# Optimization experiments

Hardware: AMD Instinct MI355X
Metric: run time of the kernel (lower is better)

The kernel has to match this reference:

```python
import jax, jax.numpy as jnp
import numpy as np

SQ, SK, D = 8192, 8192, 128

def setup_inputs() -> dict:
    k = jax.random.key(0)
    kq, kk, kv = jax.random.split(k, 3)
    query = jax.random.normal(kq, (SQ, D), dtype=jnp.float32)
    key = jax.random.normal(kk, (SK, D), dtype=jnp.float32)
    value = jax.random.normal(kv, (SK, D), dtype=jnp.float32)
    return {"query": query, "key": key, "value": value}

def reference(query, key, value):
    # attn_weights = dot_general(q, k, contract last dims) -> [Sq, Sk]
    attn_weights = jnp.einsum('qd,kd->qk', query, key)
    # softmax over key dims (second half of attn_weights dims)
    attn_weights = jax.nn.softmax(attn_weights, axis=-1)
    # dropout is identity: train=False -> deterministic
    # y = dot_general(attn_weights, value, contract key dims) -> [Sq, Dv]
    y = jnp.einsum('qk,kd->qd', attn_weights, value)
    return y
```

## Files before the change

kernel.cpp:

```cpp
#include <hip/hip_runtime.h>
#include <hip/hip_bf16.h>
#include <stdint.h>

#define SQ 8192
#define SK 8192
#define DH 128
#define L2E 1.4426950408889634f
#define CB 40.0f

typedef __attribute__((ext_vector_type(8))) _Float16 f16x8;
typedef __attribute__((ext_vector_type(8))) short bf16x8;
typedef __attribute__((ext_vector_type(16))) float f32x16;
typedef __attribute__((ext_vector_type(4))) short s16x4;
typedef __attribute__((ext_vector_type(4))) unsigned int u32x4;

__device__ __forceinline__ short f2h(float f) {
  _Float16 h = (_Float16)f;
  return __builtin_bit_cast(short, h);
}
__device__ __forceinline__ short f2bf(float f) {
  uint32_t u = __builtin_bit_cast(uint32_t, f);
  u = (u + 0x7FFFu + ((u >> 16) & 1u)) >> 16;
  return (short)u;
}

__device__ __forceinline__ void gl_lds16(const void* g, void* l) {
  __builtin_amdgcn_global_load_lds(
      (const __attribute__((address_space(1))) void*)g,
      (__attribute__((address_space(3))) void*)l, 16, 0, 0);
}

__global__ __launch_bounds__(256) void prep_kernel(const float* __restrict__ K,
                                                   const float* __restrict__ V,
                                                   short* __restrict__ Kimg,
                                                   short* __restrict__ Vimg) {
  __shared__ short T[32][136];
  const int tid = threadIdx.x;
  if (blockIdx.x < 256) {
    const int kb = blockIdx.x;
#pragma unroll
    for (int i = 0; i < 2; ++i) {
      int ci = i * 256 + tid;
      int kc = ci >> 6, lane = ci & 63;
      int key = kb * 32 + (lane & 31);
      int k0 = kc * 16 + (lane >> 5) * 8;
      const float* src = K + (size_t)key * DH + k0;
      float4 a = *(const float4*)src;
      float4 b = *(const float4*)(src + 4);
      s16x4 o0, o1;
      o0.x = f2h(a.x); o0.y = f2h(a.y); o0.z = f2h(a.z); o0.w = f2h(a.w);
      o1.x = f2h(b.x); o1.y = f2h(b.y); o1.z = f2h(b.z); o1.w = f2h(b.w);
      s16x4* dst = (s16x4*)(Kimg + (size_t)kb * 4096 + ci * 8);
      dst[0] = o0; dst[1] = o1;
    }
  } else {
    const int kb = blockIdx.x - 256;
#pragma unroll
    for (int i = 0; i < 4; ++i) {
      int fi = i * 256 + tid;
      int key = fi >> 5;
      int dc = (fi & 31) * 4;
      float4 v = ((const float4*)V)[(size_t)(kb * 32 + key) * (DH / 4) + (fi & 31)];
      T[key][dc + 0] = f2bf(v.x); T[key][dc + 1] = f2bf(v.y);
      T[key][dc + 2] = f2bf(v.z); T[key][dc + 3] = f2bf(v.w);
    }
    __syncthreads();
#pragma unroll
    for (int i = 0; i < 2; ++i) {
      int ci = i * 256 + tid;
      int lane = ci & 63;
      int g = ci >> 6;
      int dt = g & 3, ks = g >> 2;
      int base = ks * 16 + (lane >> 5) * 4;
      int d = dt * 32 + (lane & 31);
      s16x4 o0, o1;
      o0.x = T[base + 0][d]; o0.y = T[base + 1][d];
      o0.z = T[base + 2][d]; o0.w = T[base + 3][d];
      o1.x = T[base + 8][d]; o1.y = T[base + 9][d];
      o1.z = T[base + 10][d]; o1.w = T[base + 11][d];
      s16x4* dst = (s16x4*)(Vimg + (size_t)kb * 4096 + ci * 8);
      dst[0] = o0; dst[1] = o1;
    }
  }
}

#define NIT4 32
__global__ __launch_bounds__(512, 2) void attn_q128(const float* __restrict__ Q,
                                                    const short* __restrict__ Kimg,
                                                    const short* __restrict__ Vimg,
                                                    float* __restrict__ Opart,
                                                    float* __restrict__ lpart) {
  __shared__ __align__(16) char smem[98304];
  short* stg = (short*)smem;
  const int tid = threadIdx.x;
  const int w = tid >> 6;
  const int lane = tid & 63;
  const int half = lane >> 5;
  const int l32 = lane & 31;
  const int qh = w >> 1;
  const int kw = w & 1;
  const int b = blockIdx.x;
  const int kh = b & 3;
  const int qb = b >> 2;
  const int qrow0 = qb * 128 + qh * 32;
  const int kb0 = kh * 64;

  f16x8 qf[8];
  {
    const float* qp = Q + (size_t)(qrow0 + l32) * DH + half * 8;
#pragma unroll
    for (int kc = 0; kc < 8; ++kc) {
      float4 a = *(const float4*)(qp + kc * 16);
      float4 b2 = *(const float4*)(qp + kc * 16 + 4);
      f16x8 h;
      h[0] = (_Float16)a.x; h[1] = (_Float16)a.y; h[2] = (_Float16)a.z; h[3] = (_Float16)a.w;
      h[4] = (_Float16)b2.x; h[5] = (_Float16)b2.y; h[6] = (_Float16)b2.z; h[7] = (_Float16)b2.w;
      qf[kc] = h;
    }
  }

  f32x16 of[4];
#pragma unroll
  for (int dt = 0; dt < 4; ++dt)
#pragma unroll
    for (int c = 0; c < 16; ++c) of[dt][c] = 0.f;
  float l_lane = 0.f;

  const short* gsrc = (w < 4 ? Kimg : Vimg) + (size_t)kb0 * 4096 + (w & 3) * 2048 + lane * 8;
  const int ldso = ((w < 4) ? 0 : 8192) + (w & 3) * 2048;

  auto STAGE = [&](int c, int t) {
    const short* g = gsrc + (size_t)t * 8192;
    short* l = stg + c * 16384 + ldso;
#pragma unroll
    for (int j = 0; j < 4; ++j)
      gl_lds16(g + j * 512, l + j * 512);
  };

  STAGE(0, 0);
  STAGE(1, 1);
  asm volatile("s_waitcnt vmcnt(4)" ::: "memory");
  __builtin_amdgcn_s_barrier();
  __builtin_amdgcn_sched_barrier(0);

  for (int t = 0; t < NIT4; ++t) {
    const int cur = t % 3;
    const short* bk = stg + cur * 16384 + kw * 4096 + lane * 8;
    f16x8 kf[8];
#pragma unroll
    for (int kc = 0; kc < 8; ++kc) kf[kc] = *(const f16x8*)(bk + kc * 512);

    if (t + 2 < NIT4) STAGE((t + 2) % 3, t + 2);

    f32x16 sacc;
#pragma unroll
    for (int c = 0; c < 16; ++c) sacc[c] = 0.f;
#pragma unroll
    for (int kc = 0; kc < 8; ++kc)
      sacc = __builtin_amdgcn_mfma_f32_32x32x16_f16(kf[kc], qf[kc], sacc, 0, 0, 0);

    const short* bv = stg + cur * 16384 + 8192 + kw * 4096 + lane * 8;
    bf16x8 vf[8];
#pragma unroll
    for (int g2 = 0; g2 < 8; ++g2) vf[g2] = *(const bf16x8*)(bv + g2 * 512);

    u32x4 pav0, pav1;
#pragma unroll
    for (int r = 0; r < 4; ++r) {
      float pA = __builtin_amdgcn_exp2f(fmaf(sacc[2 * r], L2E, -CB));
      float pB = __builtin_amdgcn_exp2f(fmaf(sacc[2 * r + 1], L2E, -CB));
      float pC = __builtin_amdgcn_exp2f(fmaf(sacc[8 + 2 * r], L2E, -CB));
      float pD = __builtin_amdgcn_exp2f(fmaf(sacc[8 + 2 * r + 1], L2E, -CB));
      l_lane += (pA + pB) + (pC + pD);
      uint32_t uA = __builtin_bit_cast(uint32_t, pA); uA += 0x7FFFu + ((uA >> 16) & 1u);
      uint32_t uB = __builtin_bit_cast(uint32_t, pB); uB += 0x7FFFu + ((uB >> 16) & 1u);
      uint32_t uC = __builtin_bit_cast(uint32_t, pC); uC += 0x7FFFu + ((uC >> 16) & 1u);
      uint32_t uD = __builtin_bit_cast(uint32_t, pD); uD += 0x7FFFu + ((uD >> 16) & 1u);
      pav0[r] = __builtin_amdgcn_perm(uB, uA, 0x07060302u);
      pav1[r] = __builtin_amdgcn_perm(uD, uC, 0x07060302u);
    }
    bf16x8 pa0 = __builtin_bit_cast(bf16x8, pav0);
    bf16x8 pa1 = __builtin_bit_cast(bf16x8, pav1);

#pragma unroll
    for (int dt = 0; dt < 4; ++dt) {
      of[dt] = __builtin_amdgcn_mfma_f32_32x32x16_bf16(pa0, vf[dt], of[dt], 0, 0, 0);
      of[dt] = __builtin_amdgcn_mfma_f32_32x32x16_bf16(pa1, vf[4 + dt], of[dt], 0, 0, 0);
    }

    if (t + 1 < NIT4) {
      asm volatile("s_waitcnt vmcnt(4)" ::: "memory");
      __builtin_amdgcn_s_barrier();
      __builtin_amdgcn_sched_barrier(0);
    }
  }

  float l_tot = l_lane + __shfl_xor(l_lane, 32);

  __syncthreads();
  float* mO = (float*)smem;
  float* R = mO + qh * 4224;
  if (kw == 0) {
#pragma unroll
    for (int c = 0; c < 16; ++c) {
      const int row = (c & 3) + 8 * (c >> 2) + 4 * half;
      float* br = R + row * 132;
#pragma unroll
      for (int dt = 0; dt < 4; ++dt) br[dt * 32 + l32] = of[dt][c];
    }
    if (half == 0) R[l32 * 132 + 128] = l_tot;
  }
  __syncthreads();
  if (kw == 1) {
#pragma unroll
    for (int c = 0; c < 16; ++c) {
      const int row = (c & 3) + 8 * (c >> 2) + 4 * half;
      float* br = R + row * 132;
#pragma unroll
      for (int dt = 0; dt < 4; ++dt) br[dt * 32 + l32] += of[dt][c];
    }
    if (half == 0) R[l32 * 132 + 128] += l_tot;
  }
  __syncthreads();
  {
    const int row = tid >> 2;
    const int cg = tid & 3;
    const float* p = mO + (row >> 5) * 4224 + (row & 31) * 132;
    float* dst = Opart + ((size_t)kh << 20) + (size_t)(qb * 128 + row) * DH + cg * 32;
#pragma unroll
    for (int k = 0; k < 8; ++k)
      ((float4*)dst)[k] = ((const float4*)(p + cg * 32))[k];
    if (cg == 0) lpart[kh * SQ + qb * 128 + row] = p[128];
  }
}

__global__ __launch_bounds__(256) void combine4(const float* __restrict__ Opart,
                                                const float* __restrict__ lpart,
                                                float* __restrict__ out) {
  const int idx = blockIdx.x * 256 + threadIdx.x;
  const int row = idx >> 5;
  const int c4 = (idx & 31) * 4;
  const float inv = 1.f / (lpart[row] + lpart[SQ + row] +
                           lpart[2 * SQ + row] + lpart[3 * SQ + row]);
  const size_t off = (size_t)row * DH + c4;
  float4 a = *(const float4*)(Opart + off);
  const float4 b = *(const float4*)(Opart + (1u << 20) + off);
  const float4 c = *(const float4*)(Opart + (2u << 20) + off);
  const float4 d = *(const float4*)(Opart + (3u << 20) + off);
  a.x = (a.x + b.x + c.x + d.x) * inv;
  a.y = (a.y + b.y + c.y + d.y) * inv;
  a.z = (a.z + b.z + c.z + d.z) * inv;
  a.w = (a.w + b.w + c.w + d.w) * inv;
  *(float4*)(out + off) = a;
}

__global__ __launch_bounds__(512, 2) void attn_fb(const float* __restrict__ Q,
                                                  const short* __restrict__ Kimg,
                                                  const short* __restrict__ Vimg,
                                                  float* __restrict__ Oa,
                                                  float* __restrict__ Ob,
                                                  float* __restrict__ l0,
                                                  float* __restrict__ l1) {
  __shared__ __align__(16) char smem[131072];
  short* stg = (short*)smem;
  const int tid = threadIdx.x;
  const int w = tid >> 6;
  const int lane = tid & 63;
  const int half = lane >> 5;
  const int l32 = lane & 31;
  const int qh = w >> 2;
  const int ks = w & 3;
  const int qb = blockIdx.x >> 1;
  const int kh = blockIdx.x & 1;
  const int qrow0 = qb * 64 + qh * 32;
  const int kb0 = kh * 128;

  f16x8 qf[8];
  {
    const float* qp = Q + (size_t)(qrow0 + l32) * DH + half * 8;
#pragma unroll
    for (int kc = 0; kc < 8; ++kc) {
      float4 a = *(const float4*)(qp + kc * 16);
      float4 b = *(const float4*)(qp + kc * 16 + 4);
      f16x8 h;
      h[0] = (_Float16)a.x; h[1] = (_Float16)a.y; h[2] = (_Float16)a.z; h[3] = (_Float16)a.w;
      h[4] = (_Float16)b.x; h[5] = (_Float16)b.y; h[6] = (_Float16)b.z; h[7] = (_Float16)b.w;
      qf[kc] = h;
    }
  }

  f32x16 of[4];
#pragma unroll
  for (int dt = 0; dt < 4; ++dt)
#pragma unroll
    for (int c = 0; c < 16; ++c) of[dt][c] = 0.f;
  float l_lane = 0.f;

  const short* gsrc = (w < 4 ? Kimg : Vimg) + ((size_t)kb0 + ks) * 4096 + lane * 8;
  short* lbase = stg + ((w >= 4) ? 16384 : 0) + ks * 4096;

  auto STAGE = [&](int c, int t) {
    const short* g = gsrc + (size_t)t * 4 * 4096;
    short* l = lbase + c * 32768;
#pragma unroll
    for (int j = 0; j < 8; ++j)
      gl_lds16(g + j * 512, l + j * 512);
  };

  STAGE(0, 0);
  __syncthreads();
  int cur = 0;

  for (int t = 0; t < 32; ++t) {
    const short* bk = stg + cur * 16384 * 2 + ks * 4096 + lane * 8;
    f16x8 kf[8];
#pragma unroll
    for (int kc = 0; kc < 8; ++kc) kf[kc] = *(const f16x8*)(bk + kc * 512);

    if (t + 1 < 32) STAGE(cur ^ 1, t + 1);

    f32x16 sacc;
#pragma unroll
    for (int c = 0; c < 16; ++c) sacc[c] = 0.f;
#pragma unroll
    for (int kc = 0; kc < 8; ++kc)
      sacc = __builtin_amdgcn_mfma_f32_32x32x16_f16(kf[kc], qf[kc], sacc, 0, 0, 0);

    const short* bv = stg + cur * 16384 * 2 + 16384 + ks * 4096 + lane * 8;
    bf16x8 vf[8];
#pragma unroll
    for (int g2 = 0; g2 < 8; ++g2) vf[g2] = *(const bf16x8*)(bv + g2 * 512);

    u32x4 pav0, pav1;
#pragma unroll
    for (int r = 0; r < 4; ++r) {
      float pA = __builtin_amdgcn_exp2f(fmaf(sacc[2 * r], L2E, -CB));
      float pB = __builtin_amdgcn_exp2f(fmaf(sacc[2 * r + 1], L2E, -CB));
      float pC = __builtin_amdgcn_exp2f(fmaf(sacc[8 + 2 * r], L2E, -CB));
      float pD = __builtin_amdgcn_exp2f(fmaf(sacc[8 + 2 * r + 1], L2E, -CB));
      l_lane += (pA + pB) + (pC + pD);
      uint32_t uA = __builtin_bit_cast(uint32_t, pA); uA += 0x7FFFu + ((uA >> 16) & 1u);
      uint32_t uB = __builtin_bit_cast(uint32_t, pB); uB += 0x7FFFu + ((uB >> 16) & 1u);
      uint32_t uC = __builtin_bit_cast(uint32_t, pC); uC += 0x7FFFu + ((uC >> 16) & 1u);
      uint32_t uD = __builtin_bit_cast(uint32_t, pD); uD += 0x7FFFu + ((uD >> 16) & 1u);
      pav0[r] = __builtin_amdgcn_perm(uB, uA, 0x07060302u);
      pav1[r] = __builtin_amdgcn_perm(uD, uC, 0x07060302u);
    }
    bf16x8 pa0 = __builtin_bit_cast(bf16x8, pav0);
    bf16x8 pa1 = __builtin_bit_cast(bf16x8, pav1);

#pragma unroll
    for (int dt = 0; dt < 4; ++dt) {
      of[dt] = __builtin_amdgcn_mfma_f32_32x32x16_bf16(pa0, vf[dt], of[dt], 0, 0, 0);
      of[dt] = __builtin_amdgcn_mfma_f32_32x32x16_bf16(pa1, vf[4 + dt], of[dt], 0, 0, 0);
    }

    __syncthreads();
    cur ^= 1;
  }

  float l_tot = l_lane + __shfl_xor(l_lane, 32);

  __syncthreads();
  float* mO = (float*)smem;
  float* R = mO + (qh * 2 + (ks & 1)) * 4224;
  if (ks < 2) {
#pragma unroll
    for (int c = 0; c < 16; ++c) {
      const int row = (c & 3) + 8 * (c >> 2) + 4 * half;
      float* br = R + row * 132;
#pragma unroll
      for (int dt = 0; dt < 4; ++dt) br[dt * 32 + l32] = of[dt][c];
    }
    if (half == 0) R[l32 * 132 + 128] = l_tot;
  }
  __syncthreads();
  if (ks >= 2) {
#pragma unroll
    for (int c = 0; c < 16; ++c) {
      const int row = (c & 3) + 8 * (c >> 2) + 4 * half;
      float* br = R + row * 132;
#pragma unroll
      for (int dt = 0; dt < 4; ++dt) br[dt * 32 + l32] += of[dt][c];
    }
    if (half == 0) R[l32 * 132 + 128] += l_tot;
  }
  __syncthreads();
  {
    const int row = tid >> 3;
    const int cg = tid & 7;
    const int qh2 = row >> 5;
    const int r32 = row & 31;
    const float* Ra = mO + (qh2 * 2 + 0) * 4224 + r32 * 132;
    const float* Rb = mO + (qh2 * 2 + 1) * 4224 + r32 * 132;
    float lp = Ra[128] + Rb[128];
    float* dst = (kh ? Ob : Oa) + (size_t)(qb * 64 + row) * DH + cg * 16;
#pragma unroll
    for (int k = 0; k < 4; ++k) {
      float4 a = *(const float4*)(Ra + cg * 16 + k * 4);
      float4 b = *(const float4*)(Rb + cg * 16 + k * 4);
      a.x += b.x; a.y += b.y; a.z += b.z; a.w += b.w;
      *(float4*)(dst + k * 4) = a;
    }
    if (cg == 0) (kh ? l1 : l0)[qb * 64 + row] = lp;
  }
}

__global__ __launch_bounds__(256) void combine2(float* __restrict__ Oa,
                                                const float* __restrict__ Ob,
                                                const float* __restrict__ l0,
                                                const float* __restrict__ l1) {
  const int idx = blockIdx.x * 256 + threadIdx.x;
  const int row = idx >> 5;
  const int c4 = (idx & 31) * 4;
  const float inv = 1.f / (l0[row] + l1[row]);
  float* pa = Oa + (size_t)row * DH + c4;
  const float* pb = Ob + (size_t)row * DH + c4;
  float4 a = *(const float4*)pa;
  float4 b = *(const float4*)pb;
  a.x = (a.x + b.x) * inv; a.y = (a.y + b.y) * inv;
  a.z = (a.z + b.z) * inv; a.w = (a.w + b.w) * inv;
  *(float4*)pa = a;
}

extern "C" void kernel_launch(void* const* d_in, const int* in_sizes, int n_in,
                              void* d_out, int out_size, void* d_ws, size_t ws_size,
                              hipStream_t stream) {
  const float* Q = (const float*)d_in[0];
  const float* K = (const float*)d_in[1];
  const float* V = (const float*)d_in[2];
  float* out = (float*)d_out;
  char* ws = (char*)d_ws;
  short* Kimg = (short*)ws;
  short* Vimg = (short*)(ws + 2097152);
  prep_kernel<<<512, 256, 0, stream>>>(K, V, Kimg, Vimg);
  if (ws_size >= (size_t)21102592) {
    float* Opart = (float*)(ws + 4194304);
    float* lpart = (float*)(ws + 20971520);
    attn_q128<<<256, 512, 0, stream>>>(Q, Kimg, Vimg, Opart, lpart);
    combine4<<<SQ * DH / 4 / 256, 256, 0, stream>>>(Opart, lpart, out);
  } else {
    float* Ob = (float*)(ws + 4194304);
    float* l0 = (float*)(ws + 8388608);
    float* l1 = l0 + SQ;
    attn_fb<<<SQ / 64 * 2, 512, 0, stream>>>(Q, Kimg, Vimg, out, Ob, l0, l1);
    combine2<<<SQ * DH / 4 / 256, 256, 0, stream>>>(out, Ob, l0, l1);
  }
}
```

Measured before the change: 115.2 us.

## Software-pipeline QK and PV MFMAs with 4-stage LDS ring

Restructures the main attention loop so the QK^T score MFMAs for the next tile are interleaved with the PV MFMAs of the current tile. The exp/convert work now overlaps with independent matrix work instead of serialising behind it. The LDS staging ring grows from 3 to 4 buffers (128KB shared) to prefetch three tiles ahead. The K prep kernel is also changed to go through an LDS transpose for coalesced loads. The larger LDS footprint may reduce occupancy below the requested 2 blocks per CU.

```diff
diff --git a/kernel.cpp b/kernel.cpp
--- a/kernel.cpp
+++ b/kernel.cpp
@@ -39,17 +39,26 @@
   if (blockIdx.x < 256) {
     const int kb = blockIdx.x;
 #pragma unroll
+    for (int i = 0; i < 4; ++i) {
+      int fi = i * 256 + tid;
+      int key = fi >> 5;
+      int dc = (fi & 31) * 4;
+      float4 v = ((const float4*)K)[(size_t)(kb * 32 + key) * (DH / 4) + (fi & 31)];
+      T[key][dc + 0] = f2h(v.x); T[key][dc + 1] = f2h(v.y);
+      T[key][dc + 2] = f2h(v.z); T[key][dc + 3] = f2h(v.w);
+    }
+    __syncthreads();
+#pragma unroll
     for (int i = 0; i < 2; ++i) {
       int ci = i * 256 + tid;
       int kc = ci >> 6, lane = ci & 63;
-      int key = kb * 32 + (lane & 31);
+      int row = lane & 31;
       int k0 = kc * 16 + (lane >> 5) * 8;
-      const float* src = K + (size_t)key * DH + k0;
-      float4 a = *(const float4*)src;
-      float4 b = *(const float4*)(src + 4);
       s16x4 o0, o1;
-      o0.x = f2h(a.x); o0.y = f2h(a.y); o0.z = f2h(a.z); o0.w = f2h(a.w);
-      o1.x = f2h(b.x); o1.y = f2h(b.y); o1.z = f2h(b.z); o1.w = f2h(b.w);
+      o0.x = T[row][k0 + 0]; o0.y = T[row][k0 + 1];
+      o0.z = T[row][k0 + 2]; o0.w = T[row][k0 + 3];
+      o1.x = T[row][k0 + 4]; o1.y = T[row][k0 + 5];
+      o1.z = T[row][k0 + 6]; o1.w = T[row][k0 + 7];
       s16x4* dst = (s16x4*)(Kimg + (size_t)kb * 4096 + ci * 8);
       dst[0] = o0; dst[1] = o1;
     }
@@ -90,7 +99,7 @@
                                                     const short* __restrict__ Vimg,
                                                     float* __restrict__ Opart,
                                                     float* __restrict__ lpart) {
-  __shared__ __align__(16) char smem[98304];
+  __shared__ __align__(16) char smem[131072];
   short* stg = (short*)smem;
   const int tid = threadIdx.x;
   const int w = tid >> 6;
@@ -139,38 +148,46 @@
 
   STAGE(0, 0);
   STAGE(1, 1);
-  asm volatile("s_waitcnt vmcnt(4)" ::: "memory");
+  asm volatile("s_waitcnt vmcnt(0)" ::: "memory");
   __builtin_amdgcn_s_barrier();
   __builtin_amdgcn_sched_barrier(0);
+  STAGE(2, 2);
+
+  f32x16 sacc_c;
+  {
+    const short* bk = stg + kw * 4096 + lane * 8;
+    f16x8 kf0[8];
+#pragma unroll
+    for (int kc = 0; kc < 8; ++kc) kf0[kc] = *(const f16x8*)(bk + kc * 512);
+#pragma unroll
+    for (int c = 0; c < 16; ++c) sacc_c[c] = 0.f;
+#pragma unroll
+    for (int kc = 0; kc < 8; ++kc)
+      sacc_c = __builtin_amdgcn_mfma_f32_32x32x16_f16(kf0[kc], qf[kc], sacc_c, 0, 0, 0);
+  }
 
   for (int t = 0; t < NIT4; ++t) {
-    const int cur = t % 3;
-    const short* bk = stg + cur * 16384 + kw * 4096 + lane * 8;
+    const int cur = t & 3;
+    bf16x8 vf[8];
+    const short* bv = stg + cur * 16384 + 8192 + kw * 4096 + lane * 8;
+#pragma unroll
+    for (int g2 = 0; g2 < 8; ++g2) vf[g2] = *(const bf16x8*)(bv + g2 * 512);
     f16x8 kf[8];
-#pragma unroll
-    for (int kc = 0; kc < 8; ++kc) kf[kc] = *(const f16x8*)(bk + kc * 512);
-
-    if (t + 2 < NIT4) STAGE((t + 2) % 3, t + 2);
-
-    f32x16 sacc;
-#pragma unroll
-    for (int c = 0; c < 16; ++c) sacc[c] = 0.f;
-#pragma unroll
-    for (int kc = 0; kc < 8; ++kc)
-      sacc = __builtin_amdgcn_mfma_f32_32x32x16_f16(kf[kc], qf[kc], sacc, 0, 0, 0);
-
-    const short* bv = stg + cur * 16384 + 8192 + kw * 4096 + lane * 8;
-    bf16x8 vf[8];
-#pragma unroll
-    for (int g2 = 0; g2 < 8; ++g2) vf[g2] = *(const bf16x8*)(bv + g2 * 512);
+    if (t + 1 < NIT4) {
+      const short* bk = stg + ((t + 1) & 3) * 16384 + kw * 4096 + lane * 8;
+#pragma unroll
+      for (int kc = 0; kc < 8; ++kc) kf[kc] = *(const f16x8*)(bk + kc * 512);
+    }
+
+    if (t + 3 < NIT4) STAGE((t + 3) & 3, t + 3);
 
     u32x4 pav0, pav1;
 #pragma unroll
     for (int r = 0; r < 4; ++r) {
-      float pA = __builtin_amdgcn_exp2f(fmaf(sacc[2 * r], L2E, -CB));
-      float pB = __builtin_amdgcn_exp2f(fmaf(sacc[2 * r + 1], L2E, -CB));
-      float pC = __builtin_amdgcn_exp2f(fmaf(sacc[8 + 2 * r], L2E, -CB));
-      float pD = __builtin_amdgcn_exp2f(fmaf(sacc[8 + 2 * r + 1], L2E, -CB));
+      float pA = __builtin_amdgcn_exp2f(fmaf(sacc_c[2 * r], L2E, -CB));
+      float pB = __builtin_amdgcn_exp2f(fmaf(sacc_c[2 * r + 1], L2E, -CB));
+      float pC = __builtin_amdgcn_exp2f(fmaf(sacc_c[8 + 2 * r], L2E, -CB));
+      float pD = __builtin_amdgcn_exp2f(fmaf(sacc_c[8 + 2 * r + 1], L2E, -CB));
       l_lane += (pA + pB) + (pC + pD);
       uint32_t uA = __builtin_bit_cast(uint32_t, pA); uA += 0x7FFFu + ((uA >> 16) & 1u);
       uint32_t uB = __builtin_bit_cast(uint32_t, pB); uB += 0x7FFFu + ((uB >> 16) & 1u);
@@ -182,17 +199,32 @@
     bf16x8 pa0 = __builtin_bit_cast(bf16x8, pav0);
     bf16x8 pa1 = __builtin_bit_cast(bf16x8, pav1);
 
-#pragma unroll
-    for (int dt = 0; dt < 4; ++dt) {
-      of[dt] = __builtin_amdgcn_mfma_f32_32x32x16_bf16(pa0, vf[dt], of[dt], 0, 0, 0);
-      of[dt] = __builtin_amdgcn_mfma_f32_32x32x16_bf16(pa1, vf[4 + dt], of[dt], 0, 0, 0);
-    }
-
+    f32x16 sacc_n;
+#pragma unroll
+    for (int c = 0; c < 16; ++c) sacc_n[c] = 0.f;
     if (t + 1 < NIT4) {
-      asm volatile("s_waitcnt vmcnt(4)" ::: "memory");
+#pragma unroll
+      for (int i = 0; i < 4; ++i) {
+        sacc_n = __builtin_amdgcn_mfma_f32_32x32x16_f16(kf[2 * i], qf[2 * i], sacc_n, 0, 0, 0);
+        of[i] = __builtin_amdgcn_mfma_f32_32x32x16_bf16(pa0, vf[i], of[i], 0, 0, 0);
+        sacc_n = __builtin_amdgcn_mfma_f32_32x32x16_f16(kf[2 * i + 1], qf[2 * i + 1], sacc_n, 0, 0, 0);
+        of[i] = __builtin_amdgcn_mfma_f32_32x32x16_bf16(pa1, vf[4 + i], of[i], 0, 0, 0);
+      }
+    } else {
+#pragma unroll
+      for (int dt = 0; dt < 4; ++dt) {
+        of[dt] = __builtin_amdgcn_mfma_f32_32x32x16_bf16(pa0, vf[dt], of[dt], 0, 0, 0);
+        of[dt] = __builtin_amdgcn_mfma_f32_32x32x16_bf16(pa1, vf[4 + dt], of[dt], 0, 0, 0);
+      }
+    }
+
+    if (t + 1 < NIT4) {
+      if (t + 3 < NIT4) asm volatile("s_waitcnt vmcnt(4)" ::: "memory");
+      else              asm volatile("s_waitcnt vmcnt(0)" ::: "memory");
       __builtin_amdgcn_s_barrier();
       __builtin_amdgcn_sched_barrier(0);
     }
+    sacc_c = sacc_n;
   }
 
   float l_tot = l_lane + __shfl_xor(l_lane, 32);
@@ -312,7 +344,7 @@
   int cur = 0;
 
   for (int t = 0; t < 32; ++t) {
-    const short* bk = stg + cur * 16384 * 2 + ks * 4096 + lane * 8;
+    const short* bk = stg + cur * 32768 + ks * 4096 + lane * 8;
     f16x8 kf[8];
 #pragma unroll
     for (int kc = 0; kc < 8; ++kc) kf[kc] = *(const f16x8*)(bk + kc * 512);
@@ -326,7 +358,7 @@
     for (int kc = 0; kc < 8; ++kc)
       sacc = __builtin_amdgcn_mfma_f32_32x32x16_f16(kf[kc], qf[kc], sacc, 0, 0, 0);
 
-    const short* bv = stg + cur * 16384 * 2 + 16384 + ks * 4096 + lane * 8;
+    const short* bv = stg + cur * 32768 + 16384 + ks * 4096 + lane * 8;
     bf16x8 vf[8];
 #pragma unroll
     for (int g2 = 0; g2 < 8; ++g2) vf[g2] = *(const bf16x8*)(bv + g2 * 512);
```

Measured after the change: 115.3 us. Within noise of the previous version (+0.1%).

## Load K/V fragments directly from global into registers, dropping LDS staging

Applied to the files above, without the earlier changes.

The main attention kernel no longer stages K/V tiles into LDS with a triple buffer and barriers. Each wave now loads its pre-swizzled K and V fragments straight from global memory into registers, prefetching the next tile while the current MFMAs run. The change also raises wave priority around the MFMA blocks, staggers wave start with s_sleep, remaps block indices so neighbouring blocks share key ranges in cache, and makes the K prep kernel go through an LDS transpose for coalesced reads. This removes barrier and LDS traffic, but it relies on L2/MALL bandwidth and costs more registers, since each of the two waves sharing a key tile now fetches it separately.

```diff
diff --git a/kernel.cpp b/kernel.cpp
--- a/kernel.cpp
+++ b/kernel.cpp
@@ -39,17 +39,26 @@
   if (blockIdx.x < 256) {
     const int kb = blockIdx.x;
 #pragma unroll
+    for (int i = 0; i < 4; ++i) {
+      int fi = i * 256 + tid;
+      int key = fi >> 5;
+      int dc = (fi & 31) * 4;
+      float4 v = ((const float4*)K)[(size_t)(kb * 32 + key) * (DH / 4) + (fi & 31)];
+      T[key][dc + 0] = f2h(v.x); T[key][dc + 1] = f2h(v.y);
+      T[key][dc + 2] = f2h(v.z); T[key][dc + 3] = f2h(v.w);
+    }
+    __syncthreads();
+#pragma unroll
     for (int i = 0; i < 2; ++i) {
       int ci = i * 256 + tid;
       int kc = ci >> 6, lane = ci & 63;
-      int key = kb * 32 + (lane & 31);
+      int row = lane & 31;
       int k0 = kc * 16 + (lane >> 5) * 8;
-      const float* src = K + (size_t)key * DH + k0;
-      float4 a = *(const float4*)src;
-      float4 b = *(const float4*)(src + 4);
       s16x4 o0, o1;
-      o0.x = f2h(a.x); o0.y = f2h(a.y); o0.z = f2h(a.z); o0.w = f2h(a.w);
-      o1.x = f2h(b.x); o1.y = f2h(b.y); o1.z = f2h(b.z); o1.w = f2h(b.w);
+      o0.x = T[row][k0 + 0]; o0.y = T[row][k0 + 1];
+      o0.z = T[row][k0 + 2]; o0.w = T[row][k0 + 3];
+      o1.x = T[row][k0 + 4]; o1.y = T[row][k0 + 5];
+      o1.z = T[row][k0 + 6]; o1.w = T[row][k0 + 7];
       s16x4* dst = (s16x4*)(Kimg + (size_t)kb * 4096 + ci * 8);
       dst[0] = o0; dst[1] = o1;
     }
@@ -84,14 +93,13 @@
   }
 }
 
-#define NIT4 32
-__global__ __launch_bounds__(512, 2) void attn_q128(const float* __restrict__ Q,
-                                                    const short* __restrict__ Kimg,
-                                                    const short* __restrict__ Vimg,
-                                                    float* __restrict__ Opart,
-                                                    float* __restrict__ lpart) {
-  __shared__ __align__(16) char smem[98304];
-  short* stg = (short*)smem;
+#define NITD 32
+__global__ __launch_bounds__(512, 2) void attn_q128d(const float* __restrict__ Q,
+                                                     const short* __restrict__ Kimg,
+                                                     const short* __restrict__ Vimg,
+                                                     float* __restrict__ Opart,
+                                                     float* __restrict__ lpart) {
+  __shared__ __align__(16) char smem[67584];
   const int tid = threadIdx.x;
   const int w = tid >> 6;
   const int lane = tid & 63;
@@ -100,8 +108,8 @@
   const int qh = w >> 1;
   const int kw = w & 1;
   const int b = blockIdx.x;
-  const int kh = b & 3;
-  const int qb = b >> 2;
+  const int kh = (b >> 1) & 3;
+  const int qb = ((b >> 3) << 1) | (b & 1);
   const int qrow0 = qb * 128 + qh * 32;
   const int kb0 = kh * 64;
 
@@ -126,43 +134,34 @@
     for (int c = 0; c < 16; ++c) of[dt][c] = 0.f;
   float l_lane = 0.f;
 
-  const short* gsrc = (w < 4 ? Kimg : Vimg) + (size_t)kb0 * 4096 + (w & 3) * 2048 + lane * 8;
-  const int ldso = ((w < 4) ? 0 : 8192) + (w & 3) * 2048;
-
-  auto STAGE = [&](int c, int t) {
-    const short* g = gsrc + (size_t)t * 8192;
-    short* l = stg + c * 16384 + ldso;
-#pragma unroll
-    for (int j = 0; j < 4; ++j)
-      gl_lds16(g + j * 512, l + j * 512);
-  };
-
-  STAGE(0, 0);
-  STAGE(1, 1);
-  asm volatile("s_waitcnt vmcnt(4)" ::: "memory");
-  __builtin_amdgcn_s_barrier();
-  __builtin_amdgcn_sched_barrier(0);
-
-  for (int t = 0; t < NIT4; ++t) {
-    const int cur = t % 3;
-    const short* bk = stg + cur * 16384 + kw * 4096 + lane * 8;
-    f16x8 kf[8];
-#pragma unroll
-    for (int kc = 0; kc < 8; ++kc) kf[kc] = *(const f16x8*)(bk + kc * 512);
-
-    if (t + 2 < NIT4) STAGE((t + 2) % 3, t + 2);
-
+  for (int i = 0; i < w; ++i) __builtin_amdgcn_s_sleep(8);
+
+  f16x8 kf[8];
+  bf16x8 vf[8];
+  {
+    const short* kp = Kimg + (size_t)(kb0 + kw) * 4096;
+    const short* vp = Vimg + (size_t)(kb0 + kw) * 4096;
+#pragma unroll
+    for (int kc = 0; kc < 8; ++kc) kf[kc] = *(const f16x8*)(kp + kc * 512 + lane * 8);
+#pragma unroll
+    for (int g = 0; g < 8; ++g) vf[g] = *(const bf16x8*)(vp + g * 512 + lane * 8);
+  }
+
+  for (int t = 0; t < NITD; ++t) {
     f32x16 sacc;
 #pragma unroll
     for (int c = 0; c < 16; ++c) sacc[c] = 0.f;
+    __builtin_amdgcn_s_setprio(1);
 #pragma unroll
     for (int kc = 0; kc < 8; ++kc)
       sacc = __builtin_amdgcn_mfma_f32_32x32x16_f16(kf[kc], qf[kc], sacc, 0, 0, 0);
-
-    const short* bv = stg + cur * 16384 + 8192 + kw * 4096 + lane * 8;
-    bf16x8 vf[8];
-#pragma unroll
-    for (int g2 = 0; g2 < 8; ++g2) vf[g2] = *(const bf16x8*)(bv + g2 * 512);
+    __builtin_amdgcn_s_setprio(0);
+
+    if (t + 1 < NITD) {
+      const short* kp = Kimg + (size_t)(kb0 + (t + 1) * 2 + kw) * 4096;
+#pragma unroll
+      for (int kc = 0; kc < 8; ++kc) kf[kc] = *(const f16x8*)(kp + kc * 512 + lane * 8);
+    }
 
     u32x4 pav0, pav1;
 #pragma unroll
@@ -182,16 +181,18 @@
     bf16x8 pa0 = __builtin_bit_cast(bf16x8, pav0);
     bf16x8 pa1 = __builtin_bit_cast(bf16x8, pav1);
 
+    __builtin_amdgcn_s_setprio(1);
 #pragma unroll
     for (int dt = 0; dt < 4; ++dt) {
       of[dt] = __builtin_amdgcn_mfma_f32_32x32x16_bf16(pa0, vf[dt], of[dt], 0, 0, 0);
       of[dt] = __builtin_amdgcn_mfma_f32_32x32x16_bf16(pa1, vf[4 + dt], of[dt], 0, 0, 0);
     }
-
-    if (t + 1 < NIT4) {
-      asm volatile("s_waitcnt vmcnt(4)" ::: "memory");
-      __builtin_amdgcn_s_barrier();
-      __builtin_amdgcn_sched_barrier(0);
+    __builtin_amdgcn_s_setprio(0);
+
+    if (t + 1 < NITD) {
+      const short* vp = Vimg + (size_t)(kb0 + (t + 1) * 2 + kw) * 4096;
+#pragma unroll
+      for (int g = 0; g < 8; ++g) vf[g] = *(const bf16x8*)(vp + g * 512 + lane * 8);
     }
   }
 
@@ -312,7 +313,7 @@
   int cur = 0;
 
   for (int t = 0; t < 32; ++t) {
-    const short* bk = stg + cur * 16384 * 2 + ks * 4096 + lane * 8;
+    const short* bk = stg + cur * 32768 + ks * 4096 + lane * 8;
     f16x8 kf[8];
 #pragma unroll
     for (int kc = 0; kc < 8; ++kc) kf[kc] = *(const f16x8*)(bk + kc * 512);
@@ -326,7 +327,7 @@
     for (int kc = 0; kc < 8; ++kc)
       sacc = __builtin_amdgcn_mfma_f32_32x32x16_f16(kf[kc], qf[kc], sacc, 0, 0, 0);
 
-    const short* bv = stg + cur * 16384 * 2 + 16384 + ks * 4096 + lane * 8;
+    const short* bv = stg + cur * 32768 + 16384 + ks * 4096 + lane * 8;
     bf16x8 vf[8];
 #pragma unroll
     for (int g2 = 0; g2 < 8; ++g2) vf[g2] = *(const bf16x8*)(bv + g2 * 512);
@@ -437,7 +438,7 @@
   if (ws_size >= (size_t)21102592) {
     float* Opart = (float*)(ws + 4194304);
     float* lpart = (float*)(ws + 20971520);
-    attn_q128<<<256, 512, 0, stream>>>(Q, Kimg, Vimg, Opart, lpart);
+    attn_q128d<<<256, 512, 0, stream>>>(Q, Kimg, Vimg, Opart, lpart);
     combine4<<<SQ * DH / 4 / 256, 256, 0, stream>>>(Opart, lpart, out);
   } else {
     float* Ob = (float*)(ws + 4194304);
```

Measured after the change: 121.0 us. +5.1%, slower.
